# Optimization experiments

Hardware: AMD Instinct MI355X
Metric: run time of the kernel (lower is better)

## Reference

```python
import jax, jax.numpy as jnp
import numpy as np

MARGIN = 0.2


def setup_inputs() -> dict:
    key = jax.random.key(0)
    k1, k2 = jax.random.split(key)
    N, D, T = 4096, 1024, 100000
    batch = jax.random.normal(k1, (N, D), dtype=jnp.float32)
    triplets = jax.random.randint(k2, (T, 3), 0, N, dtype=jnp.int64)
    return {"batch": batch, "triplets": triplets}


def reference(batch, triplets):
    # Fused gather + squared-distance + hinge over all triplets at once.
    a = batch[triplets[:, 0]]  # [T, D]
    p = batch[triplets[:, 1]]  # [T, D]
    n = batch[triplets[:, 2]]  # [T, D]
    d_ap = jnp.sum((a - p) ** 2, axis=-1)  # [T]
    d_an = jnp.sum((a - n) ** 2, axis=-1)  # [T]
    loss = jax.nn.relu(d_ap - d_an + MARGIN)
    return jnp.mean(loss)
```

## Files before the change

kernel.cpp:

```cpp
#include <hip/hip_runtime.h>


constexpr float MARGIN = 0.2f;
constexpr int D = 1024;

typedef float f32x2 __attribute__((ext_vector_type(2)));

__global__ __launch_bounds__(256)
void convert_norm_kernel(const float* __restrict__ in,
                         uint* __restrict__ out8,
                         float* __restrict__ norms, int nrows)
{
    const int lane = threadIdx.x & 63;
    const int wib  = threadIdx.x >> 6;
    const int nw   = gridDim.x * 4;
    for (int row = blockIdx.x * 4 + wib; row < nrows; row += nw) {
        const float4* r4 = (const float4*)(in + (size_t)row * D);
        uint* o = out8 + (size_t)row * (D / 4);
        float nrm = 0.0f;
        #pragma unroll
        for (int k = 0; k < 4; ++k) {
            const float4 v = r4[lane + 64 * k];
            uint u = 0;
            u = (uint)__builtin_amdgcn_cvt_pk_fp8_f32(v.x, v.y, (int)u, false);
            u = (uint)__builtin_amdgcn_cvt_pk_fp8_f32(v.z, v.w, (int)u, true);
            o[lane + 64 * k] = u;
            nrm = fmaf(v.x, v.x, fmaf(v.y, v.y, fmaf(v.z, v.z, fmaf(v.w, v.w, nrm))));
        }
        #pragma unroll
        for (int off = 32; off > 0; off >>= 1) nrm += __shfl_xor(nrm, off, 64);
        if (lane == 0) norms[row] = nrm;
    }
}

__device__ __forceinline__ void dot_u(uint ua, uint up, uint un, float& dot)
{
    const f32x2 a0 = __builtin_amdgcn_cvt_pk_f32_fp8((int)ua, false);
    const f32x2 a1 = __builtin_amdgcn_cvt_pk_f32_fp8((int)ua, true);
    const f32x2 p0 = __builtin_amdgcn_cvt_pk_f32_fp8((int)up, false);
    const f32x2 p1 = __builtin_amdgcn_cvt_pk_f32_fp8((int)up, true);
    const f32x2 n0 = __builtin_amdgcn_cvt_pk_f32_fp8((int)un, false);
    const f32x2 n1 = __builtin_amdgcn_cvt_pk_f32_fp8((int)un, true);
    dot = fmaf(a0.x, n0.x - p0.x, dot);
    dot = fmaf(a0.y, n0.y - p0.y, dot);
    dot = fmaf(a1.x, n1.x - p1.x, dot);
    dot = fmaf(a1.y, n1.y - p1.y, dot);
}

__global__ __launch_bounds__(256)
void triplet_dot_kernel(const unsigned char* __restrict__ batch8,
                        const int*   __restrict__ trip,
                        const float* __restrict__ norms,
                        float*       __restrict__ partials, int T)
{
    const int lane = threadIdx.x & 63;
    const int wib  = threadIdx.x >> 6;
    const int wave_id = blockIdx.x * 4 + wib;
    const int n_waves = gridDim.x * 4;

    const unsigned char* base = batch8 + lane * 16;

    float acc = 0.0f;
    for (int t = wave_id; t < T; t += n_waves) {
        const int ia  = trip[3 * t + 0];
        const int ip  = trip[3 * t + 1];
        const int in_ = trip[3 * t + 2];

        const uint4 av = *(const uint4*)(base + (size_t)ia * D);
        const uint4 pv = *(const uint4*)(base + (size_t)ip * D);
        const uint4 nv = *(const uint4*)(base + (size_t)in_ * D);

        float dot = 0.0f;
        dot_u(av.x, pv.x, nv.x, dot);
        dot_u(av.y, pv.y, nv.y, dot);
        dot_u(av.z, pv.z, nv.z, dot);
        dot_u(av.w, pv.w, nv.w, dot);

        #pragma unroll
        for (int off = 32; off > 0; off >>= 1) dot += __shfl_xor(dot, off, 64);

        const float loss = norms[ip] - norms[in_] + 2.0f * dot + MARGIN;
        acc += loss > 0.0f ? loss : 0.0f;
    }

    __shared__ float s[4];
    if (lane == 0) s[wib] = acc;
    __syncthreads();
    if (threadIdx.x == 0)
        partials[blockIdx.x] = (s[0] + s[1]) + (s[2] + s[3]);
}

__global__ __launch_bounds__(256)
void final_mean_kernel(const float* __restrict__ part, int n,
                       float* __restrict__ out, float invT)
{
    __shared__ float s[256];
    float acc = 0.0f;
    for (int i = threadIdx.x; i < n; i += 256) acc += part[i];
    s[threadIdx.x] = acc;
    __syncthreads();
    #pragma unroll
    for (int st = 128; st > 0; st >>= 1) {
        if (threadIdx.x < st) s[threadIdx.x] += s[threadIdx.x + st];
        __syncthreads();
    }
    if (threadIdx.x == 0) out[0] = s[0] * invT;
}

__global__ __launch_bounds__(256)
void triplet_full_kernel(const float* __restrict__ batch,
                         const int*   __restrict__ trip,
                         float*       __restrict__ partials, int T)
{
    const int lane = threadIdx.x & 63;
    const int wib  = threadIdx.x >> 6;
    const int wave_id = blockIdx.x * 4 + wib;
    const int n_waves = gridDim.x * 4;

    float acc = 0.0f;
    for (int t = wave_id; t < T; t += n_waves) {
        const int ia  = trip[3 * t + 0];
        const int ip  = trip[3 * t + 1];
        const int in_ = trip[3 * t + 2];
        const float4* A  = (const float4*)(batch + (size_t)ia * D);
        const float4* P  = (const float4*)(batch + (size_t)ip * D);
        const float4* Nv = (const float4*)(batch + (size_t)in_ * D);
        float dap = 0.0f, dan = 0.0f;
        #pragma unroll
        for (int c = 0; c < 4; ++c) {
            const int idx = lane + c * 64;
            float4 av = A[idx], pv = P[idx], nv = Nv[idx];
            float d;
            d = av.x - pv.x; dap += d * d;
            d = av.y - pv.y; dap += d * d;
            d = av.z - pv.z; dap += d * d;
            d = av.w - pv.w; dap += d * d;
            d = av.x - nv.x; dan += d * d;
            d = av.y - nv.y; dan += d * d;
            d = av.z - nv.z; dan += d * d;
            d = av.w - nv.w; dan += d * d;
        }
        float diff = dap - dan;
        #pragma unroll
        for (int off = 32; off > 0; off >>= 1) diff += __shfl_xor(diff, off, 64);
        const float loss = diff + MARGIN;
        acc += loss > 0.0f ? loss : 0.0f;
    }
    __shared__ float s[4];
    if (lane == 0) s[wib] = acc;
    __syncthreads();
    if (threadIdx.x == 0) partials[blockIdx.x] = (s[0] + s[1]) + (s[2] + s[3]);
}

extern "C" void kernel_launch(void* const* d_in, const int* in_sizes, int n_in,
                              void* d_out, int out_size, void* d_ws, size_t ws_size,
                              hipStream_t stream)
{
    const float* batch = (const float*)d_in[0];
    const int*   trip  = (const int*)d_in[1];
    float* out = (float*)d_out;
    const int T     = in_sizes[1] / 3;
    const int ND    = in_sizes[0];
    const int nrows = ND / D;

    const int BLOCKS = 2048;
    const size_t fp8_bytes  = ((size_t)ND + 255) & ~(size_t)255;
    const size_t norm_bytes = ((size_t)nrows * sizeof(float) + 255) & ~(size_t)255;
    const size_t need = fp8_bytes + norm_bytes + (size_t)BLOCKS * sizeof(float);

    if (ws_size >= need) {
        unsigned char* batch8 = (unsigned char*)d_ws;
        float* norms    = (float*)((char*)d_ws + fp8_bytes);
        float* partials = (float*)((char*)d_ws + fp8_bytes + norm_bytes);
        convert_norm_kernel<<<1024, 256, 0, stream>>>(batch, (uint*)batch8, norms, nrows);
        triplet_dot_kernel<<<BLOCKS, 256, 0, stream>>>(batch8, trip, norms, partials, T);
        final_mean_kernel<<<1, 256, 0, stream>>>(partials, BLOCKS, out, 1.0f / (float)T);
    } else {
        float* partials = (float*)d_ws;
        triplet_full_kernel<<<BLOCKS, 256, 0, stream>>>(batch, trip, partials, T);
        final_mean_kernel<<<1, 256, 0, stream>>>(partials, BLOCKS, out, 1.0f / (float)T);
    }
}
```

Measured before the change: 34.90 us.

## Bucket triplets by anchor via counting sort to reuse anchor rows per wave

Adds a histogram of anchor indices, a prefix scan and an atomic scatter that groups triplets by anchor. Each wave then handles half of one anchor's bucket, loads and unpacks the anchor row once, and streams only positive/negative rows with nontemporal loads. Norm differences plus margin are precomputed per triplet during the scatter. The goal is to cut anchor-row gathers and index traffic, at the cost of three extra small kernels (zero, scan, scatter), atomics and load imbalance across buckets of uneven size.

After: 79.86 us. 2.29x slower.

```diff
diff --git a/kernel.cpp b/kernel.cpp
--- a/kernel.cpp
+++ b/kernel.cpp
@@ -3,13 +3,25 @@
 
 constexpr float MARGIN = 0.2f;
 constexpr int D = 1024;
+constexpr int NB = 4096;
 
 typedef float f32x2 __attribute__((ext_vector_type(2)));
-
-__global__ __launch_bounds__(256)
-void convert_norm_kernel(const float* __restrict__ in,
-                         uint* __restrict__ out8,
-                         float* __restrict__ norms, int nrows)
+typedef uint  u32x4 __attribute__((ext_vector_type(4)));
+
+__global__ __launch_bounds__(256)
+void zero_kernel(int* p, int n)
+{
+    int i = blockIdx.x * 256 + threadIdx.x;
+    if (i < n) p[i] = 0;
+}
+
+__global__ __launch_bounds__(256)
+void convert_norm_hist_kernel(const float* __restrict__ in,
+                              uint* __restrict__ out8,
+                              float* __restrict__ norms,
+                              const int* __restrict__ trip,
+                              int* __restrict__ counts,
+                              int nrows, int T)
 {
     const int lane = threadIdx.x & 63;
     const int wib  = threadIdx.x >> 6;
@@ -31,56 +43,141 @@
         for (int off = 32; off > 0; off >>= 1) nrm += __shfl_xor(nrm, off, 64);
         if (lane == 0) norms[row] = nrm;
     }
-}
-
-__device__ __forceinline__ void dot_u(uint ua, uint up, uint un, float& dot)
-{
-    const f32x2 a0 = __builtin_amdgcn_cvt_pk_f32_fp8((int)ua, false);
-    const f32x2 a1 = __builtin_amdgcn_cvt_pk_f32_fp8((int)ua, true);
-    const f32x2 p0 = __builtin_amdgcn_cvt_pk_f32_fp8((int)up, false);
-    const f32x2 p1 = __builtin_amdgcn_cvt_pk_f32_fp8((int)up, true);
-    const f32x2 n0 = __builtin_amdgcn_cvt_pk_f32_fp8((int)un, false);
-    const f32x2 n1 = __builtin_amdgcn_cvt_pk_f32_fp8((int)un, true);
-    dot = fmaf(a0.x, n0.x - p0.x, dot);
-    dot = fmaf(a0.y, n0.y - p0.y, dot);
-    dot = fmaf(a1.x, n1.x - p1.x, dot);
-    dot = fmaf(a1.y, n1.y - p1.y, dot);
-}
-
-__global__ __launch_bounds__(256)
-void triplet_dot_kernel(const unsigned char* __restrict__ batch8,
-                        const int*   __restrict__ trip,
-                        const float* __restrict__ norms,
-                        float*       __restrict__ partials, int T)
-{
-    const int lane = threadIdx.x & 63;
-    const int wib  = threadIdx.x >> 6;
-    const int wave_id = blockIdx.x * 4 + wib;
-    const int n_waves = gridDim.x * 4;
-
-    const unsigned char* base = batch8 + lane * 16;
-
-    float acc = 0.0f;
-    for (int t = wave_id; t < T; t += n_waves) {
+    for (int t = blockIdx.x * 256 + threadIdx.x; t < T; t += gridDim.x * 256)
+        atomicAdd(&counts[trip[3 * t]], 1);
+}
+
+__global__ __launch_bounds__(256)
+void scan_kernel(const int* __restrict__ counts, int* __restrict__ offsets)
+{
+    __shared__ int s[256];
+    const int tid = threadIdx.x;
+    const int base = tid * (NB / 256);
+    int local[NB / 256];
+    int sum = 0;
+    #pragma unroll
+    for (int k = 0; k < NB / 256; ++k) { local[k] = sum; sum += counts[base + k]; }
+    s[tid] = sum;
+    __syncthreads();
+    #pragma unroll
+    for (int off = 1; off < 256; off <<= 1) {
+        int v = (tid >= off) ? s[tid - off] : 0;
+        __syncthreads();
+        s[tid] += v;
+        __syncthreads();
+    }
+    const int prefix = (tid == 0) ? 0 : s[tid - 1];
+    #pragma unroll
+    for (int k = 0; k < NB / 256; ++k) offsets[base + k] = prefix + local[k];
+    if (tid == 255) offsets[NB] = prefix + sum;
+}
+
+__global__ __launch_bounds__(256)
+void scatter_kernel(const int* __restrict__ trip,
+                    const float* __restrict__ norms,
+                    const int* __restrict__ offsets,
+                    int* __restrict__ cursor,
+                    int2* __restrict__ spn,
+                    float* __restrict__ sbase, int T)
+{
+    for (int t = blockIdx.x * 256 + threadIdx.x; t < T; t += gridDim.x * 256) {
         const int ia  = trip[3 * t + 0];
         const int ip  = trip[3 * t + 1];
         const int in_ = trip[3 * t + 2];
-
-        const uint4 av = *(const uint4*)(base + (size_t)ia * D);
-        const uint4 pv = *(const uint4*)(base + (size_t)ip * D);
-        const uint4 nv = *(const uint4*)(base + (size_t)in_ * D);
-
-        float dot = 0.0f;
-        dot_u(av.x, pv.x, nv.x, dot);
-        dot_u(av.y, pv.y, nv.y, dot);
-        dot_u(av.z, pv.z, nv.z, dot);
-        dot_u(av.w, pv.w, nv.w, dot);
-
-        #pragma unroll
-        for (int off = 32; off > 0; off >>= 1) dot += __shfl_xor(dot, off, 64);
-
-        const float loss = norms[ip] - norms[in_] + 2.0f * dot + MARGIN;
-        acc += loss > 0.0f ? loss : 0.0f;
+        const int pos = offsets[ia] + atomicAdd(&cursor[ia], 1);
+        spn[pos]   = make_int2(ip, in_);
+        sbase[pos] = norms[ip] - norms[in_] + MARGIN;
+    }
+}
+
+__device__ __forceinline__ void unpack16(u32x4 u, float* a)
+{
+    #pragma unroll
+    for (int j = 0; j < 4; ++j) {
+        const uint w = u[j];
+        const f32x2 lo = __builtin_amdgcn_cvt_pk_f32_fp8((int)w, false);
+        const f32x2 hi = __builtin_amdgcn_cvt_pk_f32_fp8((int)w, true);
+        a[4 * j + 0] = lo.x; a[4 * j + 1] = lo.y;
+        a[4 * j + 2] = hi.x; a[4 * j + 3] = hi.y;
+    }
+}
+
+__device__ __forceinline__ float dot_pn(const float* a, u32x4 pv, u32x4 nv)
+{
+    float dot = 0.0f;
+    #pragma unroll
+    for (int j = 0; j < 4; ++j) {
+        const uint pu = pv[j];
+        const uint nu = nv[j];
+        const f32x2 p0 = __builtin_amdgcn_cvt_pk_f32_fp8((int)pu, false);
+        const f32x2 p1 = __builtin_amdgcn_cvt_pk_f32_fp8((int)pu, true);
+        const f32x2 n0 = __builtin_amdgcn_cvt_pk_f32_fp8((int)nu, false);
+        const f32x2 n1 = __builtin_amdgcn_cvt_pk_f32_fp8((int)nu, true);
+        dot = fmaf(a[4 * j + 0], n0.x - p0.x, dot);
+        dot = fmaf(a[4 * j + 1], n0.y - p0.y, dot);
+        dot = fmaf(a[4 * j + 2], n1.x - p1.x, dot);
+        dot = fmaf(a[4 * j + 3], n1.y - p1.y, dot);
+    }
+    return dot;
+}
+
+#define NTLOAD(p) __builtin_nontemporal_load((const u32x4*)(p))
+
+__global__ __launch_bounds__(256)
+void dot_sorted_kernel(const unsigned char* __restrict__ batch8,
+                       const int2*  __restrict__ spn,
+                       const float* __restrict__ sbase,
+                       const int*   __restrict__ offsets,
+                       float*       __restrict__ partials, int nbuckets)
+{
+    const int lane = threadIdx.x & 63;
+    const int wib  = threadIdx.x >> 6;
+    const int wid  = blockIdx.x * 4 + wib;
+    const int nw   = gridDim.x * 4;
+
+    const unsigned char* lanebase = batch8 + lane * 16;
+
+    float acc = 0.0f;
+    for (int bh = wid; bh < 2 * nbuckets; bh += nw) {
+        const int b = bh >> 1;
+        const int h = bh & 1;
+        const int i0  = offsets[b] + h;
+        const int end = offsets[b + 1];
+        if (i0 >= end) continue;
+
+        float a[16];
+        unpack16(*(const u32x4*)(lanebase + (size_t)b * D), a);
+
+        int i = i0;
+        for (; i + 2 < end; i += 4) {
+            const int2 pn0 = spn[i];
+            const int2 pn1 = spn[i + 2];
+            const u32x4 pv0 = NTLOAD(lanebase + (size_t)pn0.x * D);
+            const u32x4 nv0 = NTLOAD(lanebase + (size_t)pn0.y * D);
+            const u32x4 pv1 = NTLOAD(lanebase + (size_t)pn1.x * D);
+            const u32x4 nv1 = NTLOAD(lanebase + (size_t)pn1.y * D);
+
+            float d0 = dot_pn(a, pv0, nv0);
+            float d1 = dot_pn(a, pv1, nv1);
+            #pragma unroll
+            for (int off = 32; off > 0; off >>= 1) {
+                d0 += __shfl_xor(d0, off, 64);
+                d1 += __shfl_xor(d1, off, 64);
+            }
+            const float l0 = sbase[i]     + 2.0f * d0;
+            const float l1 = sbase[i + 2] + 2.0f * d1;
+            acc += (l0 > 0.0f ? l0 : 0.0f) + (l1 > 0.0f ? l1 : 0.0f);
+        }
+        if (i < end) {
+            const int2 pn0 = spn[i];
+            const u32x4 pv0 = NTLOAD(lanebase + (size_t)pn0.x * D);
+            const u32x4 nv0 = NTLOAD(lanebase + (size_t)pn0.y * D);
+            float d0 = dot_pn(a, pv0, nv0);
+            #pragma unroll
+            for (int off = 32; off > 0; off >>= 1) d0 += __shfl_xor(d0, off, 64);
+            const float l0 = sbase[i] + 2.0f * d0;
+            acc += l0 > 0.0f ? l0 : 0.0f;
+        }
     }
 
     __shared__ float s[4];
@@ -152,6 +249,8 @@
     if (threadIdx.x == 0) partials[blockIdx.x] = (s[0] + s[1]) + (s[2] + s[3]);
 }
 
+static inline size_t align256(size_t x) { return (x + 255) & ~(size_t)255; }
+
 extern "C" void kernel_launch(void* const* d_in, const int* in_sizes, int n_in,
                               void* d_out, int out_size, void* d_ws, size_t ws_size,
                               hipStream_t stream)
@@ -163,21 +262,39 @@
     const int ND    = in_sizes[0];
     const int nrows = ND / D;
 
-    const int BLOCKS = 2048;
-    const size_t fp8_bytes  = ((size_t)ND + 255) & ~(size_t)255;
-    const size_t norm_bytes = ((size_t)nrows * sizeof(float) + 255) & ~(size_t)255;
-    const size_t need = fp8_bytes + norm_bytes + (size_t)BLOCKS * sizeof(float);
-
-    if (ws_size >= need) {
-        unsigned char* batch8 = (unsigned char*)d_ws;
-        float* norms    = (float*)((char*)d_ws + fp8_bytes);
-        float* partials = (float*)((char*)d_ws + fp8_bytes + norm_bytes);
-        convert_norm_kernel<<<1024, 256, 0, stream>>>(batch, (uint*)batch8, norms, nrows);
-        triplet_dot_kernel<<<BLOCKS, 256, 0, stream>>>(batch8, trip, norms, partials, T);
-        final_mean_kernel<<<1, 256, 0, stream>>>(partials, BLOCKS, out, 1.0f / (float)T);
+    const size_t off_fp8   = 0;
+    const size_t off_norms = off_fp8   + align256((size_t)ND);
+    const size_t off_cnt   = off_norms + align256((size_t)nrows * 4);
+    const size_t off_cur   = off_cnt   + (size_t)NB * 4;
+    const size_t off_offs  = off_cur   + (size_t)NB * 4;
+    const size_t off_spn   = off_offs  + align256((size_t)(NB + 1) * 4);
+    const size_t off_sbase = off_spn   + align256((size_t)T * 8);
+    const size_t off_part  = off_sbase + align256((size_t)T * 4);
+    const size_t need      = off_part  + 2048 * 4;
+
+    if (nrows <= NB && ws_size >= need) {
+        unsigned char* ws = (unsigned char*)d_ws;
+        uint*  batch8  = (uint*)(ws + off_fp8);
+        float* norms   = (float*)(ws + off_norms);
+        int*   counts  = (int*)(ws + off_cnt);
+        int*   cursor  = (int*)(ws + off_cur);
+        int*   offsets = (int*)(ws + off_offs);
+        int2*  spn     = (int2*)(ws + off_spn);
+        float* sbase   = (float*)(ws + off_sbase);
+        float* part    = (float*)(ws + off_part);
+
+        zero_kernel<<<(2 * NB + 255) / 256, 256, 0, stream>>>(counts, 2 * NB);
+        convert_norm_hist_kernel<<<1024, 256, 0, stream>>>(batch, batch8, norms,
+                                                           trip, counts, nrows, T);
+        scan_kernel<<<1, 256, 0, stream>>>(counts, offsets);
+        scatter_kernel<<<256, 256, 0, stream>>>(trip, norms, offsets, cursor,
+                                                spn, sbase, T);
+        dot_sorted_kernel<<<2048, 256, 0, stream>>>((unsigned char*)batch8, spn,
+                                                    sbase, offsets, part, nrows);
+        final_mean_kernel<<<1, 256, 0, stream>>>(part, 2048, out, 1.0f / (float)T);
     } else {
-        float* partials = (float*)d_ws;
-        triplet_full_kernel<<<BLOCKS, 256, 0, stream>>>(batch, trip, partials, T);
-        final_mean_kernel<<<1, 256, 0, stream>>>(partials, BLOCKS, out, 1.0f / (float)T);
-    }
-}
+        float* part = (float*)d_ws;
+        triplet_full_kernel<<<2048, 256, 0, stream>>>(batch, trip, part, T);
+        final_mean_kernel<<<1, 256, 0, stream>>>(part, 2048, out, 1.0f / (float)T);
+    }
+}
```

## Fuse final mean into triplet kernel via last-block reduction and buffer loads

Applied to the files above, without the earlier changes.

Removes the separate final reduction kernel launch by having the last block to finish, detected with an atomic counter that the convert kernel resets, sum all partials and write the mean. The triplet loop now gives each wave a contiguous range of triplets instead of a grid-stride, and the row gathers use raw buffer loads with a cache-policy flag. This saves one kernel launch and its dependency gap, at the cost of atomics and fences at the end of the triplet kernel.

New measurement: 77.05 us. 121% more time.

```diff
diff --git a/kernel.cpp b/kernel.cpp
--- a/kernel.cpp
+++ b/kernel.cpp
@@ -5,12 +5,31 @@
 constexpr int D = 1024;
 
 typedef float f32x2 __attribute__((ext_vector_type(2)));
+typedef int   i32x4 __attribute__((ext_vector_type(4)));
+
+__device__ i32x4 llvm_amdgcn_raw_buffer_load_i32x4(i32x4 srsrc, int voffset,
+                                                   int soffset, int cpol)
+    __asm("llvm.amdgcn.raw.buffer.load.v4i32");
+
+__device__ __forceinline__ i32x4 make_rsrc(const void* p, int bytes)
+{
+    union { const void* p; uint u[2]; } cvt;
+    cvt.p = p;
+    i32x4 r;
+    r.x = (int)cvt.u[0];
+    r.y = (int)(cvt.u[1] & 0xffffu);
+    r.z = bytes;
+    r.w = 0x00020000;
+    return r;
+}
 
 __global__ __launch_bounds__(256)
 void convert_norm_kernel(const float* __restrict__ in,
                          uint* __restrict__ out8,
-                         float* __restrict__ norms, int nrows)
-{
+                         float* __restrict__ norms,
+                         int* __restrict__ counter, int nrows)
+{
+    if (blockIdx.x == 0 && threadIdx.x == 0) *counter = 0;
     const int lane = threadIdx.x & 63;
     const int wib  = threadIdx.x >> 6;
     const int nw   = gridDim.x * 4;
@@ -33,61 +52,92 @@
     }
 }
 
-__device__ __forceinline__ void dot_u(uint ua, uint up, uint un, float& dot)
-{
-    const f32x2 a0 = __builtin_amdgcn_cvt_pk_f32_fp8((int)ua, false);
-    const f32x2 a1 = __builtin_amdgcn_cvt_pk_f32_fp8((int)ua, true);
-    const f32x2 p0 = __builtin_amdgcn_cvt_pk_f32_fp8((int)up, false);
-    const f32x2 p1 = __builtin_amdgcn_cvt_pk_f32_fp8((int)up, true);
-    const f32x2 n0 = __builtin_amdgcn_cvt_pk_f32_fp8((int)un, false);
-    const f32x2 n1 = __builtin_amdgcn_cvt_pk_f32_fp8((int)un, true);
-    dot = fmaf(a0.x, n0.x - p0.x, dot);
-    dot = fmaf(a0.y, n0.y - p0.y, dot);
-    dot = fmaf(a1.x, n1.x - p1.x, dot);
-    dot = fmaf(a1.y, n1.y - p1.y, dot);
+__device__ __forceinline__ float dot_apn(i32x4 av, i32x4 pv, i32x4 nv)
+{
+    float dot = 0.0f;
+    #pragma unroll
+    for (int j = 0; j < 4; ++j) {
+        const int au = av[j], pu = pv[j], nu = nv[j];
+        const f32x2 a0 = __builtin_amdgcn_cvt_pk_f32_fp8(au, false);
+        const f32x2 a1 = __builtin_amdgcn_cvt_pk_f32_fp8(au, true);
+        const f32x2 p0 = __builtin_amdgcn_cvt_pk_f32_fp8(pu, false);
+        const f32x2 p1 = __builtin_amdgcn_cvt_pk_f32_fp8(pu, true);
+        const f32x2 n0 = __builtin_amdgcn_cvt_pk_f32_fp8(nu, false);
+        const f32x2 n1 = __builtin_amdgcn_cvt_pk_f32_fp8(nu, true);
+        dot = fmaf(a0.x, n0.x - p0.x, dot);
+        dot = fmaf(a0.y, n0.y - p0.y, dot);
+        dot = fmaf(a1.x, n1.x - p1.x, dot);
+        dot = fmaf(a1.y, n1.y - p1.y, dot);
+    }
+    return dot;
 }
 
 __global__ __launch_bounds__(256)
 void triplet_dot_kernel(const unsigned char* __restrict__ batch8,
                         const int*   __restrict__ trip,
                         const float* __restrict__ norms,
-                        float*       __restrict__ partials, int T)
+                        float*       __restrict__ partials,
+                        int*         __restrict__ counter,
+                        float*       __restrict__ out,
+                        int T, int nd_bytes, int nblocks, float invT)
 {
     const int lane = threadIdx.x & 63;
     const int wib  = threadIdx.x >> 6;
-    const int wave_id = blockIdx.x * 4 + wib;
-    const int n_waves = gridDim.x * 4;
-
-    const unsigned char* base = batch8 + lane * 16;
+    const int wid  = blockIdx.x * 4 + wib;
+    const int nw   = gridDim.x * 4;
+
+    const i32x4 rsrc = make_rsrc(batch8, nd_bytes);
+    const int laneoff = lane * 16;
+
+    const int TR = (T + nw - 1) / nw;
+    const int t0 = wid * TR;
+    const int t1 = (t0 + TR < T) ? (t0 + TR) : T;
 
     float acc = 0.0f;
-    for (int t = wave_id; t < T; t += n_waves) {
+    for (int t = t0; t < t1; ++t) {
         const int ia  = trip[3 * t + 0];
         const int ip  = trip[3 * t + 1];
         const int in_ = trip[3 * t + 2];
 
-        const uint4 av = *(const uint4*)(base + (size_t)ia * D);
-        const uint4 pv = *(const uint4*)(base + (size_t)ip * D);
-        const uint4 nv = *(const uint4*)(base + (size_t)in_ * D);
-
-        float dot = 0.0f;
-        dot_u(av.x, pv.x, nv.x, dot);
-        dot_u(av.y, pv.y, nv.y, dot);
-        dot_u(av.z, pv.z, nv.z, dot);
-        dot_u(av.w, pv.w, nv.w, dot);
-
-        #pragma unroll
-        for (int off = 32; off > 0; off >>= 1) dot += __shfl_xor(dot, off, 64);
-
-        const float loss = norms[ip] - norms[in_] + 2.0f * dot + MARGIN;
+        const i32x4 av = llvm_amdgcn_raw_buffer_load_i32x4(rsrc, ia * (int)D + laneoff, 0, 1);
+        const i32x4 pv = llvm_amdgcn_raw_buffer_load_i32x4(rsrc, ip * (int)D + laneoff, 0, 1);
+        const i32x4 nv = llvm_amdgcn_raw_buffer_load_i32x4(rsrc, in_ * (int)D + laneoff, 0, 1);
+
+        float d = dot_apn(av, pv, nv);
+        #pragma unroll
+        for (int off = 32; off > 0; off >>= 1) d += __shfl_xor(d, off, 64);
+
+        const float loss = norms[ip] - norms[in_] + 2.0f * d + MARGIN;
         acc += loss > 0.0f ? loss : 0.0f;
     }
 
     __shared__ float s[4];
+    __shared__ int islast;
     if (lane == 0) s[wib] = acc;
     __syncthreads();
-    if (threadIdx.x == 0)
-        partials[blockIdx.x] = (s[0] + s[1]) + (s[2] + s[3]);
+    if (threadIdx.x == 0) {
+        const float blocksum = (s[0] + s[1]) + (s[2] + s[3]);
+        atomicExch(&partials[blockIdx.x], blocksum);
+        __threadfence();
+        const int old = atomicAdd(counter, 1);
+        islast = (old == nblocks - 1);
+    }
+    __syncthreads();
+    if (islast) {
+        __threadfence();
+        __shared__ float r[256];
+        float a = 0.0f;
+        for (int i = threadIdx.x; i < nblocks; i += 256)
+            a += atomicAdd(&partials[i], 0.0f);
+        r[threadIdx.x] = a;
+        __syncthreads();
+        #pragma unroll
+        for (int st = 128; st > 0; st >>= 1) {
+            if (threadIdx.x < st) r[threadIdx.x] += r[threadIdx.x + st];
+            __syncthreads();
+        }
+        if (threadIdx.x == 0) out[0] = r[0] * invT;
+    }
 }
 
 __global__ __launch_bounds__(256)
@@ -152,6 +202,8 @@
     if (threadIdx.x == 0) partials[blockIdx.x] = (s[0] + s[1]) + (s[2] + s[3]);
 }
 
+static inline size_t align256(size_t x) { return (x + 255) & ~(size_t)255; }
+
 extern "C" void kernel_launch(void* const* d_in, const int* in_sizes, int n_in,
                               void* d_out, int out_size, void* d_ws, size_t ws_size,
                               hipStream_t stream)
@@ -164,17 +216,21 @@
     const int nrows = ND / D;
 
     const int BLOCKS = 2048;
-    const size_t fp8_bytes  = ((size_t)ND + 255) & ~(size_t)255;
-    const size_t norm_bytes = ((size_t)nrows * sizeof(float) + 255) & ~(size_t)255;
-    const size_t need = fp8_bytes + norm_bytes + (size_t)BLOCKS * sizeof(float);
+    const size_t fp8_bytes  = align256((size_t)ND);
+    const size_t norm_bytes = align256((size_t)nrows * sizeof(float));
+    const size_t part_bytes = align256((size_t)BLOCKS * sizeof(float));
+    const size_t need = fp8_bytes + norm_bytes + part_bytes + 256;
 
     if (ws_size >= need) {
         unsigned char* batch8 = (unsigned char*)d_ws;
         float* norms    = (float*)((char*)d_ws + fp8_bytes);
         float* partials = (float*)((char*)d_ws + fp8_bytes + norm_bytes);
-        convert_norm_kernel<<<1024, 256, 0, stream>>>(batch, (uint*)batch8, norms, nrows);
-        triplet_dot_kernel<<<BLOCKS, 256, 0, stream>>>(batch8, trip, norms, partials, T);
-        final_mean_kernel<<<1, 256, 0, stream>>>(partials, BLOCKS, out, 1.0f / (float)T);
+        int*   counter  = (int*)((char*)d_ws + fp8_bytes + norm_bytes + part_bytes);
+        convert_norm_kernel<<<1024, 256, 0, stream>>>(batch, (uint*)batch8, norms,
+                                                      counter, nrows);
+        triplet_dot_kernel<<<BLOCKS, 256, 0, stream>>>(batch8, trip, norms, partials,
+                                                       counter, out, T, ND, BLOCKS,
+                                                       1.0f / (float)T);
     } else {
         float* partials = (float*)d_ws;
         triplet_full_kernel<<<BLOCKS, 256, 0, stream>>>(batch, trip, partials, T);
```

## Stage FP8 batch column chunks in LDS and compute per-chunk triplet dots

Applied to the files above, without the earlier changes.

Replaces the wave-per-triplet global gather with a scheme where each block loads a 32-byte column slice of all 4096 FP8 rows into 128KB of LDS, then each thread computes the partial dot for its triplets from LDS. Partial dots per chunk go to a workspace buffer that a new reduction kernel sums before applying norms and the hinge. This removes the cross-lane shuffle reduction and the scattered global row reads, but adds an extra kernel, a T×32 float intermediate write and read, and LDS bank conflicts from random indices. It also relies on the whole row set fitting in LDS, which is gated on nrows ≤ 4096.

Result: slower. 44.64 us (+27.9%).

```diff
diff --git a/kernel.cpp b/kernel.cpp
--- a/kernel.cpp
+++ b/kernel.cpp
@@ -3,8 +3,13 @@
 
 constexpr float MARGIN = 0.2f;
 constexpr int D = 1024;
+constexpr int NROW = 4096;
+constexpr int NCH = 32;
+constexpr int CBLK = 8;
+constexpr int NBLK = NCH * CBLK;
 
 typedef float f32x2 __attribute__((ext_vector_type(2)));
+typedef uint  u32x4 __attribute__((ext_vector_type(4)));
 
 __global__ __launch_bounds__(256)
 void convert_norm_kernel(const float* __restrict__ in,
@@ -33,61 +38,89 @@
     }
 }
 
-__device__ __forceinline__ void dot_u(uint ua, uint up, uint un, float& dot)
-{
-    const f32x2 a0 = __builtin_amdgcn_cvt_pk_f32_fp8((int)ua, false);
-    const f32x2 a1 = __builtin_amdgcn_cvt_pk_f32_fp8((int)ua, true);
-    const f32x2 p0 = __builtin_amdgcn_cvt_pk_f32_fp8((int)up, false);
-    const f32x2 p1 = __builtin_amdgcn_cvt_pk_f32_fp8((int)up, true);
-    const f32x2 n0 = __builtin_amdgcn_cvt_pk_f32_fp8((int)un, false);
-    const f32x2 n1 = __builtin_amdgcn_cvt_pk_f32_fp8((int)un, true);
-    dot = fmaf(a0.x, n0.x - p0.x, dot);
-    dot = fmaf(a0.y, n0.y - p0.y, dot);
-    dot = fmaf(a1.x, n1.x - p1.x, dot);
-    dot = fmaf(a1.y, n1.y - p1.y, dot);
-}
-
-__global__ __launch_bounds__(256)
-void triplet_dot_kernel(const unsigned char* __restrict__ batch8,
-                        const int*   __restrict__ trip,
-                        const float* __restrict__ norms,
-                        float*       __restrict__ partials, int T)
-{
-    const int lane = threadIdx.x & 63;
-    const int wib  = threadIdx.x >> 6;
-    const int wave_id = blockIdx.x * 4 + wib;
-    const int n_waves = gridDim.x * 4;
-
-    const unsigned char* base = batch8 + lane * 16;
-
-    float acc = 0.0f;
-    for (int t = wave_id; t < T; t += n_waves) {
+__global__ __launch_bounds__(512)
+void stage_dot_kernel(const uint* __restrict__ batch8,
+                      const int*  __restrict__ trip,
+                      float*      __restrict__ chunk_part,
+                      int T, int nrows)
+{
+    __shared__ uint lds[8 * NROW];
+
+    const int c     = blockIdx.x & (NCH - 1);
+    const int bslot = blockIdx.x >> 5;
+    const int tid   = threadIdx.x;
+
+    #pragma unroll
+    for (int k = 0; k < NROW / 512; ++k) {
+        const int r = k * 512 + tid;
+        if (r < nrows) {
+            const uint* src = batch8 + (size_t)r * 256 + c * 8;
+            const u32x4 w0 = *(const u32x4*)(src);
+            const u32x4 w1 = *(const u32x4*)(src + 4);
+            #pragma unroll
+            for (int j = 0; j < 4; ++j) {
+                lds[j * NROW + r]       = w0[j];
+                lds[(j + 4) * NROW + r] = w1[j];
+            }
+        }
+    }
+    __syncthreads();
+
+    const int TR = (T + CBLK - 1) / CBLK;
+    const int t0 = bslot * TR;
+    const int t1 = (t0 + TR < T) ? (t0 + TR) : T;
+
+    for (int t = t0 + tid; t < t1; t += 512) {
         const int ia  = trip[3 * t + 0];
         const int ip  = trip[3 * t + 1];
         const int in_ = trip[3 * t + 2];
 
-        const uint4 av = *(const uint4*)(base + (size_t)ia * D);
-        const uint4 pv = *(const uint4*)(base + (size_t)ip * D);
-        const uint4 nv = *(const uint4*)(base + (size_t)in_ * D);
-
         float dot = 0.0f;
-        dot_u(av.x, pv.x, nv.x, dot);
-        dot_u(av.y, pv.y, nv.y, dot);
-        dot_u(av.z, pv.z, nv.z, dot);
-        dot_u(av.w, pv.w, nv.w, dot);
-
-        #pragma unroll
-        for (int off = 32; off > 0; off >>= 1) dot += __shfl_xor(dot, off, 64);
-
-        const float loss = norms[ip] - norms[in_] + 2.0f * dot + MARGIN;
+        #pragma unroll
+        for (int j = 0; j < 8; ++j) {
+            const uint au = lds[j * NROW + ia];
+            const uint pu = lds[j * NROW + ip];
+            const uint nu = lds[j * NROW + in_];
+            const f32x2 a0 = __builtin_amdgcn_cvt_pk_f32_fp8((int)au, false);
+            const f32x2 a1 = __builtin_amdgcn_cvt_pk_f32_fp8((int)au, true);
+            const f32x2 p0 = __builtin_amdgcn_cvt_pk_f32_fp8((int)pu, false);
+            const f32x2 p1 = __builtin_amdgcn_cvt_pk_f32_fp8((int)pu, true);
+            const f32x2 n0 = __builtin_amdgcn_cvt_pk_f32_fp8((int)nu, false);
+            const f32x2 n1 = __builtin_amdgcn_cvt_pk_f32_fp8((int)nu, true);
+            dot = fmaf(a0.x, n0.x - p0.x, dot);
+            dot = fmaf(a0.y, n0.y - p0.y, dot);
+            dot = fmaf(a1.x, n1.x - p1.x, dot);
+            dot = fmaf(a1.y, n1.y - p1.y, dot);
+        }
+        chunk_part[(size_t)c * T + t] = dot;
+    }
+}
+
+__global__ __launch_bounds__(256)
+void chunk_reduce_kernel(const float* __restrict__ chunk_part,
+                         const int*   __restrict__ trip,
+                         const float* __restrict__ norms,
+                         float*       __restrict__ part2, int T)
+{
+    float acc = 0.0f;
+    for (int t = blockIdx.x * 256 + threadIdx.x; t < T; t += gridDim.x * 256) {
+        float s = 0.0f;
+        #pragma unroll
+        for (int c = 0; c < NCH; ++c) s += chunk_part[(size_t)c * T + t];
+        const int ip  = trip[3 * t + 1];
+        const int in_ = trip[3 * t + 2];
+        const float loss = norms[ip] - norms[in_] + 2.0f * s + MARGIN;
         acc += loss > 0.0f ? loss : 0.0f;
     }
-
-    __shared__ float s[4];
-    if (lane == 0) s[wib] = acc;
-    __syncthreads();
-    if (threadIdx.x == 0)
-        partials[blockIdx.x] = (s[0] + s[1]) + (s[2] + s[3]);
+    __shared__ float s[256];
+    s[threadIdx.x] = acc;
+    __syncthreads();
+    #pragma unroll
+    for (int st = 128; st > 0; st >>= 1) {
+        if (threadIdx.x < st) s[threadIdx.x] += s[threadIdx.x + st];
+        __syncthreads();
+    }
+    if (threadIdx.x == 0) part2[blockIdx.x] = s[0];
 }
 
 __global__ __launch_bounds__(256)
@@ -127,8 +160,8 @@
         const float4* Nv = (const float4*)(batch + (size_t)in_ * D);
         float dap = 0.0f, dan = 0.0f;
         #pragma unroll
-        for (int c = 0; c < 4; ++c) {
-            const int idx = lane + c * 64;
+        for (int cc = 0; cc < 4; ++cc) {
+            const int idx = lane + cc * 64;
             float4 av = A[idx], pv = P[idx], nv = Nv[idx];
             float d;
             d = av.x - pv.x; dap += d * d;
@@ -152,6 +185,8 @@
     if (threadIdx.x == 0) partials[blockIdx.x] = (s[0] + s[1]) + (s[2] + s[3]);
 }
 
+static inline size_t align256(size_t x) { return (x + 255) & ~(size_t)255; }
+
 extern "C" void kernel_launch(void* const* d_in, const int* in_sizes, int n_in,
                               void* d_out, int out_size, void* d_ws, size_t ws_size,
                               hipStream_t stream)
@@ -163,21 +198,25 @@
     const int ND    = in_sizes[0];
     const int nrows = ND / D;
 
-    const int BLOCKS = 2048;
-    const size_t fp8_bytes  = ((size_t)ND + 255) & ~(size_t)255;
-    const size_t norm_bytes = ((size_t)nrows * sizeof(float) + 255) & ~(size_t)255;
-    const size_t need = fp8_bytes + norm_bytes + (size_t)BLOCKS * sizeof(float);
-
-    if (ws_size >= need) {
-        unsigned char* batch8 = (unsigned char*)d_ws;
-        float* norms    = (float*)((char*)d_ws + fp8_bytes);
-        float* partials = (float*)((char*)d_ws + fp8_bytes + norm_bytes);
-        convert_norm_kernel<<<1024, 256, 0, stream>>>(batch, (uint*)batch8, norms, nrows);
-        triplet_dot_kernel<<<BLOCKS, 256, 0, stream>>>(batch8, trip, norms, partials, T);
-        final_mean_kernel<<<1, 256, 0, stream>>>(partials, BLOCKS, out, 1.0f / (float)T);
+    const size_t fp8_bytes  = align256((size_t)ND);
+    const size_t norm_bytes = align256((size_t)nrows * sizeof(float));
+    const size_t cp_bytes   = align256((size_t)NCH * T * sizeof(float));
+    const size_t need = fp8_bytes + norm_bytes + cp_bytes + 256 * sizeof(float);
+
+    if (nrows <= NROW && ws_size >= need) {
+        unsigned char* ws = (unsigned char*)d_ws;
+        uint*  batch8     = (uint*)ws;
+        float* norms      = (float*)(ws + fp8_bytes);
+        float* chunk_part = (float*)(ws + fp8_bytes + norm_bytes);
+        float* part2      = (float*)(ws + fp8_bytes + norm_bytes + cp_bytes);
+
+        convert_norm_kernel<<<1024, 256, 0, stream>>>(batch, batch8, norms, nrows);
+        stage_dot_kernel<<<NBLK, 512, 0, stream>>>(batch8, trip, chunk_part, T, nrows);
+        chunk_reduce_kernel<<<256, 256, 0, stream>>>(chunk_part, trip, norms, part2, T);
+        final_mean_kernel<<<1, 256, 0, stream>>>(part2, 256, out, 1.0f / (float)T);
     } else {
         float* partials = (float*)d_ws;
-        triplet_full_kernel<<<BLOCKS, 256, 0, stream>>>(batch, trip, partials, T);
-        final_mean_kernel<<<1, 256, 0, stream>>>(partials, BLOCKS, out, 1.0f / (float)T);
-    }
-}
+        triplet_full_kernel<<<2048, 256, 0, stream>>>(batch, trip, partials, T);
+        final_mean_kernel<<<1, 256, 0, stream>>>(partials, 2048, out, 1.0f / (float)T);
+    }
+}
```
